# Kernel tuning notes

Hardware: AMD Instinct MI355X
Metric: run time of the kernel (lower is better)

The kernel has to match this reference:

```python
import jax, jax.numpy as jnp
import numpy as np

D_MODEL = 1024
NUM_HEADS = 16
D_K = D_MODEL // NUM_HEADS


def setup_inputs() -> dict:
    key = jax.random.key(0)
    ks = jax.random.split(key, 11)
    B, S = 2, 2048
    scale = 1.0 / np.sqrt(D_MODEL)
    inp = {
        "query": jax.random.normal(ks[0], (B, S, D_MODEL), jnp.float32),
        "key": jax.random.normal(ks[1], (B, S, D_MODEL), jnp.float32),
        "value": jax.random.normal(ks[2], (B, S, D_MODEL), jnp.float32),
        "Wq": jax.random.normal(ks[3], (D_MODEL, D_MODEL), jnp.float32) * scale,
        "bq": jnp.zeros((D_MODEL,), jnp.float32),
        "Wk": jax.random.normal(ks[4], (D_MODEL, D_MODEL), jnp.float32) * scale,
        "bk": jnp.zeros((D_MODEL,), jnp.float32),
        "Wv": jax.random.normal(ks[5], (D_MODEL, D_MODEL), jnp.float32) * scale,
        "bv": jnp.zeros((D_MODEL,), jnp.float32),
        "Wo": jax.random.normal(ks[6], (D_MODEL, D_MODEL), jnp.float32) * scale,
        "bo": jnp.zeros((D_MODEL,), jnp.float32),
    }
    return inp


def _split_heads(x):
    B, S, _ = x.shape
    return x.reshape(B, S, NUM_HEADS, D_K).transpose(0, 2, 1, 3)  # [B,H,S,d_k]


def reference(query, key, value, Wq, bq, Wk, bk, Wv, bv, Wo, bo):
    # Linear projections (torch Linear: x @ W.T + b)
    q = _split_heads(query @ Wq.T + bq)
    k = _split_heads(key @ Wk.T + bk)
    v = _split_heads(value @ Wv.T + bv)
    scores = jnp.einsum("bhqd,bhkd->bhqk", q, k) / jnp.sqrt(jnp.float32(D_K))
    probs = jax.nn.softmax(scores, axis=-1)
    out = jnp.einsum("bhqk,bhkd->bhqd", probs, v)  # [B,H,S,d_k]
    B, H, S, _ = out.shape
    out = out.transpose(0, 2, 1, 3).reshape(B, S, D_MODEL)
    return out @ Wo.T + bo
```

## Files before the change

kernel.cpp:

```cpp
#include <hip/hip_runtime.h>

#define D_MODEL 1024
#define NHEADS  16
#define DK      64
#define SEQ     2048
#define NBATCH  2
#define MTOT    (NBATCH * SEQ)

typedef _Float16 f16;
typedef _Float16 f16x4 __attribute__((ext_vector_type(4)));
typedef _Float16 f16x8 __attribute__((ext_vector_type(8)));
typedef float    f32x4 __attribute__((ext_vector_type(4)));

__global__ __launch_bounds__(256) void cvt_f32_to_f16(
    const float* __restrict__ q, const float* __restrict__ k, const float* __restrict__ v,
    const float* __restrict__ wq, const float* __restrict__ wk,
    const float* __restrict__ wv, const float* __restrict__ wo,
    f16* __restrict__ qf, f16* __restrict__ kf, f16* __restrict__ vf,
    f16* __restrict__ wqh, f16* __restrict__ wkh, f16* __restrict__ wvh, f16* __restrict__ woh)
{
    const int z = blockIdx.y;
    const float* src; f16* dst; int n4;
    if (z == 0)      { src = q;  dst = qf;  n4 = MTOT * D_MODEL / 4; }
    else if (z == 1) { src = k;  dst = kf;  n4 = MTOT * D_MODEL / 4; }
    else if (z == 2) { src = v;  dst = vf;  n4 = MTOT * D_MODEL / 4; }
    else if (z == 3) { src = wq; dst = wqh; n4 = D_MODEL * D_MODEL / 4; }
    else if (z == 4) { src = wk; dst = wkh; n4 = D_MODEL * D_MODEL / 4; }
    else if (z == 5) { src = wv; dst = wvh; n4 = D_MODEL * D_MODEL / 4; }
    else             { src = wo; dst = woh; n4 = D_MODEL * D_MODEL / 4; }
    for (int i = blockIdx.x * 256 + threadIdx.x; i < n4; i += gridDim.x * 256) {
        float4 t = ((const float4*)src)[i];
        f16x4 o = {(f16)t.x, (f16)t.y, (f16)t.z, (f16)t.w};
        ((f16x4*)dst)[i] = o;
    }
}

__device__ __forceinline__ void gemm128_core(
    const f16* __restrict__ A, const f16* __restrict__ Wm,
    int m0, int n0, f32x4 (&acc)[4][4])
{
    __shared__ __align__(16) f16 As[4096];
    __shared__ __align__(16) f16 Bs[4096];

    const int t    = threadIdx.x;
    const int lane = t & 63;
    const int w    = t >> 6;
    const int quad = lane >> 4, l15 = lane & 15;
    const int wr   = w >> 1,    wc  = w & 1;

    size_t offA[2], offB[2];
#pragma unroll
    for (int jj = 0; jj < 2; ++jj) {
        int s  = (w * 2 + jj) * 64 + lane;
        int ko = s >> 7, m = s & 127;
        offA[jj] = (size_t)(m0 + m) * D_MODEL + ko * 8;
        offB[jj] = (size_t)(n0 + m) * D_MODEL + ko * 8;
    }
    const int jb = __builtin_amdgcn_readfirstlane(w * 2 * 512);

#pragma unroll
    for (int i = 0; i < 4; ++i)
#pragma unroll
        for (int j = 0; j < 4; ++j) acc[i][j] = (f32x4){0.f, 0.f, 0.f, 0.f};

    auto* ldsA = (__attribute__((address_space(3))) f16*)As;
    auto* ldsB = (__attribute__((address_space(3))) f16*)Bs;

    for (int k0 = 0; k0 < D_MODEL; k0 += 32) {
#pragma unroll
        for (int jj = 0; jj < 2; ++jj) {
            __builtin_amdgcn_global_load_lds(
                (const __attribute__((address_space(1))) void*)(A + offA[jj] + k0),
                (__attribute__((address_space(3))) void*)(ldsA + jb + jj * 512),
                16, 0, 0);
            __builtin_amdgcn_global_load_lds(
                (const __attribute__((address_space(1))) void*)(Wm + offB[jj] + k0),
                (__attribute__((address_space(3))) void*)(ldsB + jb + jj * 512),
                16, 0, 0);
        }
        __syncthreads();

        f16x8 af[4], bf[4];
#pragma unroll
        for (int i = 0; i < 4; ++i) {
            af[i] = *(const f16x8*)&As[quad * 1024 + (wr * 64 + i * 16 + l15) * 8];
            bf[i] = *(const f16x8*)&Bs[quad * 1024 + (wc * 64 + i * 16 + l15) * 8];
        }
#pragma unroll
        for (int i = 0; i < 4; ++i)
#pragma unroll
            for (int j = 0; j < 4; ++j)
                acc[i][j] = __builtin_amdgcn_mfma_f32_16x16x32_f16(af[i], bf[j], acc[i][j], 0, 0, 0);
        __syncthreads();
    }
}

__global__ __launch_bounds__(256, 3) void qkv_gemm(
    const f16* __restrict__ Qf, const f16* __restrict__ Kf, const f16* __restrict__ Vf,
    const f16* __restrict__ Wqh, const f16* __restrict__ Wkh, const f16* __restrict__ Wvh,
    const float* __restrict__ bq, const float* __restrict__ bk, const float* __restrict__ bv,
    f16* __restrict__ Qh, f16* __restrict__ Kh, f16* __restrict__ Vt)
{
    const int z = blockIdx.z;
    const f16*   A    = z == 0 ? Qf  : z == 1 ? Kf  : Vf;
    const f16*   Wm   = z == 0 ? Wqh : z == 1 ? Wkh : Wvh;
    const float* bias = z == 0 ? bq  : z == 1 ? bk  : bv;

    const int m0 = blockIdx.y * 128, n0 = blockIdx.x * 128;
    f32x4 acc[4][4];
    gemm128_core(A, Wm, m0, n0, acc);

    const int t = threadIdx.x, lane = t & 63, w = t >> 6;
    const int quad = lane >> 4, l15 = lane & 15;
    const int wr = w >> 1, wc = w & 1;

    if (z < 2) {
        f16* Out = z == 0 ? Qh : Kh;
        const float sc = z == 0 ? 0.125f : 1.0f;
#pragma unroll
        for (int j = 0; j < 4; ++j) {
            const int col = n0 + wc * 64 + j * 16 + l15;
            const float bc = bias[col];
#pragma unroll
            for (int i = 0; i < 4; ++i)
#pragma unroll
                for (int r = 0; r < 4; ++r) {
                    const int row = m0 + wr * 64 + i * 16 + quad * 4 + r;
                    Out[(size_t)row * D_MODEL + col] = (f16)((acc[i][j][r] + bc) * sc);
                }
        }
    } else {
#pragma unroll
        for (int j = 0; j < 4; ++j) {
            const int col = n0 + wc * 64 + j * 16 + l15;
            const float bc = bias[col];
            const int h = col >> 6, d = col & 63;
#pragma unroll
            for (int i = 0; i < 4; ++i)
#pragma unroll
                for (int r = 0; r < 4; ++r) {
                    const int row = m0 + wr * 64 + i * 16 + quad * 4 + r;
                    const int bb = row >> 11, s = row & (SEQ - 1);
                    Vt[(size_t)((bb * NHEADS + h) * DK + d) * SEQ + s] = (f16)(acc[i][j][r] + bc);
                }
        }
    }
}

__global__ __launch_bounds__(256, 3) void oproj_gemm(
    const f16* __restrict__ A, const f16* __restrict__ Wm,
    const float* __restrict__ bias, float* __restrict__ Out)
{
    const int m0 = blockIdx.y * 128, n0 = blockIdx.x * 128;
    f32x4 acc[4][4];
    gemm128_core(A, Wm, m0, n0, acc);

    const int t = threadIdx.x, lane = t & 63, w = t >> 6;
    const int quad = lane >> 4, l15 = lane & 15;
    const int wr = w >> 1, wc = w & 1;
#pragma unroll
    for (int j = 0; j < 4; ++j) {
        const int col = n0 + wc * 64 + j * 16 + l15;
        const float bc = bias[col];
#pragma unroll
        for (int i = 0; i < 4; ++i)
#pragma unroll
            for (int r = 0; r < 4; ++r) {
                const int row = m0 + wr * 64 + i * 16 + quad * 4 + r;
                Out[(size_t)row * D_MODEL + col] = acc[i][j][r] + bc;
            }
    }
}

__device__ __forceinline__ float dpp_max16(float v) {
    v = fmaxf(v, __uint_as_float(__builtin_amdgcn_update_dpp(
            0, (int)__float_as_uint(v), 0xB1, 0xF, 0xF, false)));
    v = fmaxf(v, __uint_as_float(__builtin_amdgcn_update_dpp(
            0, (int)__float_as_uint(v), 0x4E, 0xF, 0xF, false)));
    v = fmaxf(v, __uint_as_float(__builtin_amdgcn_update_dpp(
            0, (int)__float_as_uint(v), 0x141, 0xF, 0xF, false)));
    v = fmaxf(v, __uint_as_float(__builtin_amdgcn_update_dpp(
            0, (int)__float_as_uint(v), 0x140, 0xF, 0xF, false)));
    return v;
}

__global__ __launch_bounds__(256, 2) void mha_mfma_v3(
    const f16* __restrict__ Qh, const f16* __restrict__ Kh,
    const f16* __restrict__ Vt, f16* __restrict__ Og)
{
    __shared__ __align__(16) f16 Ks[4096];
    __shared__ __align__(16) f16 Vc[4096];
    __shared__ __align__(16) f16 Ps[128 * 68];

    const int t    = threadIdx.x;
    const int w    = t >> 6;
    const int lane = t & 63;
    const int quad = lane >> 4, l15 = lane & 15;

    const int qt = blockIdx.x, bh = blockIdx.y;
    const int b  = bh >> 4,    h  = bh & 15;
    const int q0 = qt * 128;

    f16x8 aQ[2][2];
#pragma unroll
    for (int s = 0; s < 2; ++s)
#pragma unroll
        for (int c = 0; c < 2; ++c)
            aQ[s][c] = *(const f16x8*)&Qh[
                (size_t)(b * SEQ + q0 + w * 32 + s * 16 + l15) * D_MODEL
                + h * DK + c * 32 + quad * 8];

    const f16* gK[2]; const f16* gV[2]; int ldst[2];
#pragma unroll
    for (int jj = 0; jj < 2; ++jj) {
        const int kc = w * 2 + jj;
        gK[jj] = Kh + (size_t)(b * SEQ + lane) * D_MODEL + h * DK + kc * 8;
        gV[jj] = Vt + (size_t)(bh * DK + lane) * SEQ + kc * 8;
        ldst[jj] = __builtin_amdgcn_readfirstlane(kc * 512);
    }
    auto* ldsK = (__attribute__((address_space(3))) f16*)Ks;
    auto* ldsV = (__attribute__((address_space(3))) f16*)Vc;

    const f16x8 onesB = {(f16)1.f, (f16)1.f, (f16)1.f, (f16)1.f,
                         (f16)1.f, (f16)1.f, (f16)1.f, (f16)1.f};

    f32x4 o[2][4];
#pragma unroll
    for (int s = 0; s < 2; ++s)
#pragma unroll
        for (int j = 0; j < 4; ++j) o[s][j] = (f32x4){0.f, 0.f, 0.f, 0.f};
    f32x4 sacc[2] = {(f32x4){0.f, 0.f, 0.f, 0.f}, (f32x4){0.f, 0.f, 0.f, 0.f}};
    float m_run[2][4];
#pragma unroll
    for (int s = 0; s < 2; ++s)
#pragma unroll
        for (int r = 0; r < 4; ++r) m_run[s][r] = -1e30f;

    for (int kt = 0; kt < SEQ / 64; ++kt) {
#pragma unroll
        for (int jj = 0; jj < 2; ++jj) {
            __builtin_amdgcn_global_load_lds(
                (const __attribute__((address_space(1))) void*)(gK[jj] + (size_t)kt * 64 * D_MODEL),
                (__attribute__((address_space(3))) void*)(ldsK + ldst[jj]), 16, 0, 0);
            __builtin_amdgcn_global_load_lds(
                (const __attribute__((address_space(1))) void*)(gV[jj] + kt * 64),
                (__attribute__((address_space(3))) void*)(ldsV + ldst[jj]), 16, 0, 0);
        }
        __syncthreads();

        f16x8 bK[4][2], bV[4][2];
#pragma unroll
        for (int f = 0; f < 4; ++f)
#pragma unroll
            for (int c = 0; c < 2; ++c) {
                const int slot = ((c * 4 + quad) * 64 + f * 16 + l15) * 8;
                bK[f][c] = *(const f16x8*)&Ks[slot];
                bV[f][c] = *(const f16x8*)&Vc[slot];
            }

#pragma unroll
        for (int s = 0; s < 2; ++s) {
            f32x4 sc[4];
#pragma unroll
            for (int f = 0; f < 4; ++f) {
                f32x4 a = (f32x4){0.f, 0.f, 0.f, 0.f};
                a = __builtin_amdgcn_mfma_f32_16x16x32_f16(aQ[s][0], bK[f][0], a, 0, 0, 0);
                a = __builtin_amdgcn_mfma_f32_16x16x32_f16(aQ[s][1], bK[f][1], a, 0, 0, 0);
                sc[f] = a;
            }

            float al[4];
#pragma unroll
            for (int r = 0; r < 4; ++r) {
                float mt = fmaxf(fmaxf(sc[0][r], sc[1][r]), fmaxf(sc[2][r], sc[3][r]));
                mt = dpp_max16(mt);
                const float mn = fmaxf(m_run[s][r], mt);
                al[r] = __expf(m_run[s][r] - mn);
                m_run[s][r] = mn;
#pragma unroll
                for (int f = 0; f < 4; ++f) sc[f][r] = __expf(sc[f][r] - mn);
                sacc[s][r] *= al[r];
#pragma unroll
                for (int j = 0; j < 4; ++j) o[s][j][r] *= al[r];
            }

#pragma unroll
            for (int f = 0; f < 4; ++f)
#pragma unroll
                for (int r = 0; r < 4; ++r)
                    Ps[(w * 32 + s * 16 + quad * 4 + r) * 68 + f * 16 + l15] = (f16)sc[f][r];

            f16x8 aP[2];
#pragma unroll
            for (int c = 0; c < 2; ++c) {
                const int off = (w * 32 + s * 16 + l15) * 68 + c * 32 + quad * 8;
                f16x4 lo = *(const f16x4*)&Ps[off];
                f16x4 hi = *(const f16x4*)&Ps[off + 4];
                aP[c] = __builtin_shufflevector(lo, hi, 0, 1, 2, 3, 4, 5, 6, 7);
            }

#pragma unroll
            for (int j = 0; j < 4; ++j) {
                o[s][j] = __builtin_amdgcn_mfma_f32_16x16x32_f16(aP[0], bV[j][0], o[s][j], 0, 0, 0);
                o[s][j] = __builtin_amdgcn_mfma_f32_16x16x32_f16(aP[1], bV[j][1], o[s][j], 0, 0, 0);
            }
            sacc[s] = __builtin_amdgcn_mfma_f32_16x16x32_f16(aP[0], onesB, sacc[s], 0, 0, 0);
            sacc[s] = __builtin_amdgcn_mfma_f32_16x16x32_f16(aP[1], onesB, sacc[s], 0, 0, 0);
        }
        __syncthreads();
    }

#pragma unroll
    for (int s = 0; s < 2; ++s)
#pragma unroll
        for (int r = 0; r < 4; ++r) {
            const float inv = 1.f / sacc[s][r];
            const size_t row = (size_t)(b * SEQ + q0 + w * 32 + s * 16 + quad * 4 + r) * D_MODEL
                               + h * DK;
#pragma unroll
            for (int j = 0; j < 4; ++j)
                Og[row + j * 16 + l15] = (f16)(o[s][j][r] * inv);
        }
}

extern "C" void kernel_launch(void* const* d_in, const int* in_sizes, int n_in,
                              void* d_out, int out_size, void* d_ws, size_t ws_size,
                              hipStream_t stream)
{
    const float* query = (const float*)d_in[0];
    const float* key   = (const float*)d_in[1];
    const float* value = (const float*)d_in[2];
    const float* Wq    = (const float*)d_in[3];
    const float* bq    = (const float*)d_in[4];
    const float* Wk    = (const float*)d_in[5];
    const float* bk    = (const float*)d_in[6];
    const float* Wv    = (const float*)d_in[7];
    const float* bv    = (const float*)d_in[8];
    const float* Wo    = (const float*)d_in[9];
    const float* bo    = (const float*)d_in[10];
    float* out = (float*)d_out;

    f16* Qf  = (f16*)d_ws;
    f16* Kf  = Qf  + (size_t)MTOT * D_MODEL;
    f16* Vf  = Kf  + (size_t)MTOT * D_MODEL;
    f16* Wqh = Vf  + (size_t)MTOT * D_MODEL;
    f16* Wkh = Wqh + (size_t)D_MODEL * D_MODEL;
    f16* Wvh = Wkh + (size_t)D_MODEL * D_MODEL;
    f16* Woh = Wvh + (size_t)D_MODEL * D_MODEL;
    f16* Qh  = Woh + (size_t)D_MODEL * D_MODEL;
    f16* Kh  = Qh  + (size_t)MTOT * D_MODEL;
    f16* Vt  = Kh  + (size_t)MTOT * D_MODEL;
    f16* ATh = Vt  + (size_t)MTOT * D_MODEL;

    cvt_f32_to_f16<<<dim3(1024, 7), 256, 0, stream>>>(
        query, key, value, Wq, Wk, Wv, Wo, Qf, Kf, Vf, Wqh, Wkh, Wvh, Woh);

    qkv_gemm<<<dim3(D_MODEL / 128, MTOT / 128, 3), 256, 0, stream>>>(
        Qf, Kf, Vf, Wqh, Wkh, Wvh, bq, bk, bv, Qh, Kh, Vt);

    mha_mfma_v3<<<dim3(SEQ / 128, NBATCH * NHEADS), 256, 0, stream>>>(Qh, Kh, Vt, ATh);

    oproj_gemm<<<dim3(D_MODEL / 128, MTOT / 128), 256, 0, stream>>>(ATh, Woh, bo, out);
}
```

Baseline: 289.2 us.

## Split-K output projection, smaller attention blocks, and exp2 softmax

The output projection now splits K into two halves, writing fp32 partials into reused workspace buffers, and a separate reduce kernel adds the partials and the bias. The attention kernel moves from 128-query blocks of 256 threads to 64-query blocks of 128 threads, doubling the grid for better occupancy and CU coverage. Softmax now uses exp2, with log2e folded into the Q scaling. The cost is an extra fp32 partial write and read pass plus one more kernel launch.

```diff
diff --git a/kernel.cpp b/kernel.cpp
--- a/kernel.cpp
+++ b/kernel.cpp
@@ -11,6 +11,8 @@
 typedef _Float16 f16x4 __attribute__((ext_vector_type(4)));
 typedef _Float16 f16x8 __attribute__((ext_vector_type(8)));
 typedef float    f32x4 __attribute__((ext_vector_type(4)));
+
+#define LOG2E 1.44269504088896340736f
 
 __global__ __launch_bounds__(256) void cvt_f32_to_f16(
     const float* __restrict__ q, const float* __restrict__ k, const float* __restrict__ v,
@@ -37,7 +39,7 @@
 
 __device__ __forceinline__ void gemm128_core(
     const f16* __restrict__ A, const f16* __restrict__ Wm,
-    int m0, int n0, f32x4 (&acc)[4][4])
+    int m0, int n0, int kbeg, int kend, f32x4 (&acc)[4][4])
 {
     __shared__ __align__(16) f16 As[4096];
     __shared__ __align__(16) f16 Bs[4096];
@@ -66,7 +68,7 @@
     auto* ldsA = (__attribute__((address_space(3))) f16*)As;
     auto* ldsB = (__attribute__((address_space(3))) f16*)Bs;
 
-    for (int k0 = 0; k0 < D_MODEL; k0 += 32) {
+    for (int k0 = kbeg; k0 < kend; k0 += 32) {
 #pragma unroll
         for (int jj = 0; jj < 2; ++jj) {
             __builtin_amdgcn_global_load_lds(
@@ -108,7 +110,7 @@
 
     const int m0 = blockIdx.y * 128, n0 = blockIdx.x * 128;
     f32x4 acc[4][4];
-    gemm128_core(A, Wm, m0, n0, acc);
+    gemm128_core(A, Wm, m0, n0, 0, D_MODEL, acc);
 
     const int t = threadIdx.x, lane = t & 63, w = t >> 6;
     const int quad = lane >> 4, l15 = lane & 15;
@@ -116,7 +118,7 @@
 
     if (z < 2) {
         f16* Out = z == 0 ? Qh : Kh;
-        const float sc = z == 0 ? 0.125f : 1.0f;
+        const float sc = z == 0 ? 0.125f * LOG2E : 1.0f;
 #pragma unroll
         for (int j = 0; j < 4; ++j) {
             const int col = n0 + wc * 64 + j * 16 + l15;
@@ -147,28 +149,44 @@
     }
 }
 
-__global__ __launch_bounds__(256, 3) void oproj_gemm(
+__global__ __launch_bounds__(256, 3) void oproj_splitk(
     const f16* __restrict__ A, const f16* __restrict__ Wm,
-    const float* __restrict__ bias, float* __restrict__ Out)
-{
+    float* __restrict__ P0, float* __restrict__ P1)
+{
+    const int z = blockIdx.z;
     const int m0 = blockIdx.y * 128, n0 = blockIdx.x * 128;
     f32x4 acc[4][4];
-    gemm128_core(A, Wm, m0, n0, acc);
-
+    gemm128_core(A, Wm, m0, n0, z * 512, z * 512 + 512, acc);
+
+    float* Out = z == 0 ? P0 : P1;
     const int t = threadIdx.x, lane = t & 63, w = t >> 6;
     const int quad = lane >> 4, l15 = lane & 15;
     const int wr = w >> 1, wc = w & 1;
 #pragma unroll
     for (int j = 0; j < 4; ++j) {
         const int col = n0 + wc * 64 + j * 16 + l15;
-        const float bc = bias[col];
 #pragma unroll
         for (int i = 0; i < 4; ++i)
 #pragma unroll
             for (int r = 0; r < 4; ++r) {
                 const int row = m0 + wr * 64 + i * 16 + quad * 4 + r;
-                Out[(size_t)row * D_MODEL + col] = acc[i][j][r] + bc;
-            }
+                Out[(size_t)row * D_MODEL + col] = acc[i][j][r];
+            }
+    }
+}
+
+__global__ __launch_bounds__(256) void reduce_bias(
+    const float* __restrict__ P0, const float* __restrict__ P1,
+    const float* __restrict__ bias, float* __restrict__ Out)
+{
+    const int n4 = MTOT * D_MODEL / 4;
+    for (int i = blockIdx.x * 256 + threadIdx.x; i < n4; i += gridDim.x * 256) {
+        float4 a = ((const float4*)P0)[i];
+        float4 b = ((const float4*)P1)[i];
+        float4 c = ((const float4*)bias)[i & 255];
+        float4 o = {a.x + b.x + c.x, a.y + b.y + c.y,
+                    a.z + b.z + c.z, a.w + b.w + c.w};
+        ((float4*)Out)[i] = o;
     }
 }
 
@@ -184,13 +202,13 @@
     return v;
 }
 
-__global__ __launch_bounds__(256, 2) void mha_mfma_v3(
+__global__ __launch_bounds__(128, 2) void mha_mfma_v4(
     const f16* __restrict__ Qh, const f16* __restrict__ Kh,
     const f16* __restrict__ Vt, f16* __restrict__ Og)
 {
     __shared__ __align__(16) f16 Ks[4096];
     __shared__ __align__(16) f16 Vc[4096];
-    __shared__ __align__(16) f16 Ps[128 * 68];
+    __shared__ __align__(16) f16 Ps[64 * 68];
 
     const int t    = threadIdx.x;
     const int w    = t >> 6;
@@ -199,7 +217,7 @@
 
     const int qt = blockIdx.x, bh = blockIdx.y;
     const int b  = bh >> 4,    h  = bh & 15;
-    const int q0 = qt * 128;
+    const int q0 = qt * 64;
 
     f16x8 aQ[2][2];
 #pragma unroll
@@ -210,10 +228,10 @@
                 (size_t)(b * SEQ + q0 + w * 32 + s * 16 + l15) * D_MODEL
                 + h * DK + c * 32 + quad * 8];
 
-    const f16* gK[2]; const f16* gV[2]; int ldst[2];
-#pragma unroll
-    for (int jj = 0; jj < 2; ++jj) {
-        const int kc = w * 2 + jj;
+    const f16* gK[4]; const f16* gV[4]; int ldst[4];
+#pragma unroll
+    for (int jj = 0; jj < 4; ++jj) {
+        const int kc = w * 4 + jj;
         gK[jj] = Kh + (size_t)(b * SEQ + lane) * D_MODEL + h * DK + kc * 8;
         gV[jj] = Vt + (size_t)(bh * DK + lane) * SEQ + kc * 8;
         ldst[jj] = __builtin_amdgcn_readfirstlane(kc * 512);
@@ -238,7 +256,7 @@
 
     for (int kt = 0; kt < SEQ / 64; ++kt) {
 #pragma unroll
-        for (int jj = 0; jj < 2; ++jj) {
+        for (int jj = 0; jj < 4; ++jj) {
             __builtin_amdgcn_global_load_lds(
                 (const __attribute__((address_space(1))) void*)(gK[jj] + (size_t)kt * 64 * D_MODEL),
                 (__attribute__((address_space(3))) void*)(ldsK + ldst[jj]), 16, 0, 0);
@@ -275,10 +293,10 @@
                 float mt = fmaxf(fmaxf(sc[0][r], sc[1][r]), fmaxf(sc[2][r], sc[3][r]));
                 mt = dpp_max16(mt);
                 const float mn = fmaxf(m_run[s][r], mt);
-                al[r] = __expf(m_run[s][r] - mn);
+                al[r] = __builtin_exp2f(m_run[s][r] - mn);
                 m_run[s][r] = mn;
 #pragma unroll
-                for (int f = 0; f < 4; ++f) sc[f][r] = __expf(sc[f][r] - mn);
+                for (int f = 0; f < 4; ++f) sc[f][r] = __builtin_exp2f(sc[f][r] - mn);
                 sacc[s][r] *= al[r];
 #pragma unroll
                 for (int j = 0; j < 4; ++j) o[s][j][r] *= al[r];
@@ -351,6 +369,8 @@
     f16* Kh  = Qh  + (size_t)MTOT * D_MODEL;
     f16* Vt  = Kh  + (size_t)MTOT * D_MODEL;
     f16* ATh = Vt  + (size_t)MTOT * D_MODEL;
+    float* P0 = (float*)Qf;
+    float* P1 = (float*)Qh;
 
     cvt_f32_to_f16<<<dim3(1024, 7), 256, 0, stream>>>(
         query, key, value, Wq, Wk, Wv, Wo, Qf, Kf, Vf, Wqh, Wkh, Wvh, Woh);
@@ -358,7 +378,9 @@
     qkv_gemm<<<dim3(D_MODEL / 128, MTOT / 128, 3), 256, 0, stream>>>(
         Qf, Kf, Vf, Wqh, Wkh, Wvh, bq, bk, bv, Qh, Kh, Vt);
 
-    mha_mfma_v3<<<dim3(SEQ / 128, NBATCH * NHEADS), 256, 0, stream>>>(Qh, Kh, Vt, ATh);
-
-    oproj_gemm<<<dim3(D_MODEL / 128, MTOT / 128), 256, 0, stream>>>(ATh, Woh, bo, out);
-}
+    mha_mfma_v4<<<dim3(SEQ / 64, NBATCH * NHEADS), 128, 0, stream>>>(Qh, Kh, Vt, ATh);
+
+    oproj_splitk<<<dim3(D_MODEL / 128, MTOT / 128, 2), 256, 0, stream>>>(ATh, Woh, P0, P1);
+
+    reduce_bias<<<dim3(1024), 256, 0, stream>>>(P0, P1, bo, out);
+}
```

Result: slower. 314.1 us (+8.6%).
